# Kernel tuning notes

Hardware: AMD Instinct MI355X
Metric: run time of the kernel (lower is better)

The kernel has to match this reference:

```python
import jax, jax.numpy as jnp
import numpy as np

B, L, F, H, N_HASHES = 2, 2048, 1024, 16, 4
HD = F // H  # head_dim = 64


def setup_inputs() -> dict:
    key = jax.random.key(0)
    ks = jax.random.split(key, 8)
    s = 0.02
    return {
        "x": jax.random.normal(ks[0], (B, L, F), jnp.float32),
        "Wqk": jax.random.normal(ks[1], (F, 2 * F), jnp.float32) * s,
        "bqk": jnp.zeros((2 * F,), jnp.float32),
        "Wv": jax.random.normal(ks[2], (F, F), jnp.float32) * s,
        "bv": jnp.zeros((F,), jnp.float32),
        "Wo": jax.random.normal(ks[3], (F, F), jnp.float32) * s,
        "bo": jnp.zeros((F,), jnp.float32),
        "R": jax.random.normal(ks[4], (H, N_HASHES, HD), jnp.float32) * s,
    }


def reference(x, Wqk, bqk, Wv, bv, Wo, bo, R):
    b, l, f = x.shape
    h, _, hd = R.shape

    qk = x @ Wqk + bqk                      # [B,L,2F]
    q, k = jnp.split(qk, 2, axis=-1)
    v = x @ Wv + bv                         # [B,L,F]

    def to_heads(t):
        return t.reshape(b, l, h, hd).transpose(0, 2, 1, 3)  # [B,H,L,D]

    q, k, v = to_heads(q), to_heads(k), to_heads(v)

    # LSH hashing of queries: argmax over [rotated, -rotated]
    rotated = jnp.einsum('bhld,hrd->bhlr', q, R)             # [B,H,L,n_hashes]
    buckets = jnp.argmax(jnp.concatenate([rotated, -rotated], axis=-1), axis=-1)  # [B,H,L]

    # Sort sequence positions by bucket id (per batch/head)
    idx = jnp.argsort(buckets, axis=-1)                      # [B,H,L]

    def gather_l(t):
        return jnp.take_along_axis(t, idx[..., None], axis=2)

    sq, sk, sv = gather_l(q), gather_l(k), gather_l(v)

    # Full dense attention over the sorted sequence
    scale = 1.0 / np.sqrt(hd).astype(np.float32)
    dots = jnp.einsum('bhqd,bhkd->bhqk', sq, sk) * scale     # [B,H,L,L]
    attn = jax.nn.softmax(dots, axis=-1)
    out = jnp.einsum('bhqk,bhkd->bhqd', attn, sv)            # [B,H,L,D]

    # Scatter back to original order
    restore = jnp.argsort(idx, axis=-1)
    out = jnp.take_along_axis(out, restore[..., None], axis=2)
    out = out.transpose(0, 2, 1, 3).reshape(b, l, f)
    return out @ Wo + bo
```

## Files before the change

kernel.cpp:

```cpp
#include <hip/hip_runtime.h>


#define B_ 2
#define L_ 2048
#define F_ 1024
#define H_ 16
#define D_ 64
#define M_ 4096

typedef unsigned short u16;
typedef unsigned int   u32;
typedef __bf16 bf16x8 __attribute__((ext_vector_type(8)));
typedef float  f32x4  __attribute__((ext_vector_type(4)));

__device__ __forceinline__ u16 f2bf(float f) {
    __bf16 h = (__bf16)f;
    return __builtin_bit_cast(u16, h);
}

__device__ __forceinline__ void glds16(const void* g, void* l) {
    __builtin_amdgcn_global_load_lds(
        (const __attribute__((address_space(1))) u32*)g,
        (__attribute__((address_space(3))) u32*)l, 16, 0, 0);
}

#define MFMA16(a, b, c) __builtin_amdgcn_mfma_f32_16x16x32_bf16(a, b, c, 0, 0, 0)

__global__ __launch_bounds__(256) void cast_x(const float* __restrict__ x, u16* __restrict__ xb) {
    int i0 = blockIdx.x * 256 + threadIdx.x;
    #pragma unroll
    for (int r = 0; r < 4; ++r) {
        int i = i0 + r * 262144;
        float4 v = ((const float4*)x)[i];
        ushort4 o; o.x = f2bf(v.x); o.y = f2bf(v.y); o.z = f2bf(v.z); o.w = f2bf(v.w);
        ((ushort4*)xb)[i] = o;
    }
}

__global__ __launch_bounds__(256) void tr_all(
    const float* __restrict__ Wqk, const float* __restrict__ Wv,
    const float* __restrict__ Wo, u16* __restrict__ Wt, u16* __restrict__ Wot)
{
    __shared__ float tile[32][33];
    const int z = blockIdx.z;
    const float* src; u16* dst; int N;
    if (z == 0)      { src = Wqk; dst = Wt;                       N = 2048; }
    else if (z == 1) { src = Wv;  dst = Wt + (size_t)2048 * 1024; N = 1024; }
    else             { src = Wo;  dst = Wot;                      N = 1024; }
    int n0 = blockIdx.x * 32, k0 = blockIdx.y * 32;
    if (n0 >= N) return;
    int tx = threadIdx.x & 31, ty = threadIdx.x >> 5;
    #pragma unroll
    for (int i = 0; i < 4; ++i) {
        int k = ty + i * 8;
        tile[k][tx] = src[(size_t)(k0 + k) * N + n0 + tx];
    }
    __syncthreads();
    #pragma unroll
    for (int i = 0; i < 4; ++i) {
        int n = ty + i * 8;
        dst[(size_t)(n0 + n) * 1024 + k0 + tx] = f2bf(tile[tx][n]);
    }
}

__device__ __forceinline__ void gemm_loop(
    const u16* __restrict__ A, const u16* __restrict__ Bt,
    size_t m0, size_t n0, u16* As, u16* Bs, int t, f32x4 acc[4][4])
{
    const int w = t >> 6, lane = t & 63, ml = lane & 15, quad = lane >> 4;
    const int mw = (w >> 1) * 64, nw = (w & 1) * 64;
    const int srow = (lane >> 2), schunk = (lane & 3) * 8;

    for (int k0 = 0; k0 < 1024; k0 += 32) {
        __syncthreads();
        #pragma unroll
        for (int i = 0; i < 2; ++i) {
            int row = w * 32 + i * 16 + srow;
            glds16(A  + (m0 + row) * 1024 + k0 + schunk, As + (w * 32 + i * 16) * 32);
            glds16(Bt + (n0 + row) * 1024 + k0 + schunk, Bs + (w * 32 + i * 16) * 32);
        }
        __syncthreads();
        bf16x8 af[4], bf_[4];
        #pragma unroll
        for (int mt = 0; mt < 4; ++mt)
            af[mt] = *(const bf16x8*)(As + (mw + mt * 16 + ml) * 32 + quad * 8);
        #pragma unroll
        for (int nt = 0; nt < 4; ++nt)
            bf_[nt] = *(const bf16x8*)(Bs + (nw + nt * 16 + ml) * 32 + quad * 8);
        #pragma unroll
        for (int mt = 0; mt < 4; ++mt)
            #pragma unroll
            for (int nt = 0; nt < 4; ++nt)
                acc[mt][nt] = MFMA16(af[mt], bf_[nt], acc[mt][nt]);
    }
}

__global__ __launch_bounds__(256) void qkv_gemm(
    const u16* __restrict__ xb, const u16* __restrict__ Wt,
    const float* __restrict__ bqk, const float* __restrict__ bv,
    u16* __restrict__ Qb, u16* __restrict__ Kb, u16* __restrict__ Vt)
{
    __shared__ __align__(16) u16 As[128 * 32];
    __shared__ __align__(16) u16 Bs[128 * 32];
    const int t = threadIdx.x;
    const size_t m0 = blockIdx.y * 128, n0 = blockIdx.x * 128;
    f32x4 acc[4][4] = {};
    gemm_loop(xb, Wt, m0, n0, As, Bs, t, acc);

    const int w = t >> 6, lane = t & 63, ml = lane & 15, quad = lane >> 4;
    const int mw = (w >> 1) * 64, nw = (w & 1) * 64;
    const int seg = (int)(n0 >> 10);

    #pragma unroll
    for (int mt = 0; mt < 4; ++mt) {
        #pragma unroll
        for (int nt = 0; nt < 4; ++nt) {
            f32x4 a = acc[mt][nt];
            int c = (int)n0 + nw + nt * 16 + ml;
            int mbase = (int)m0 + mw + mt * 16 + quad * 4;
            if (seg == 2) {
                int cv = c - 2048, h = cv >> 6, d = cv & 63;
                float bias = bv[cv];
                int bb = mbase >> 11, l0 = mbase & (L_ - 1);
                int g = (l0 >> 2) & 15;
                int col = (l0 & ~63) + ((g & 8) << 2) + ((g & 3) << 3) + (g & 4);
                ushort4 pk;
                pk.x = f2bf(a[0] + bias); pk.y = f2bf(a[1] + bias);
                pk.z = f2bf(a[2] + bias); pk.w = f2bf(a[3] + bias);
                *(ushort4*)&Vt[(((size_t)(bb * H_ + h)) * D_ + d) * L_ + col] = pk;
            } else {
                float bias = bqk[c];
                float sc = (seg == 0) ? 0.1803368801111244f : 1.0f;
                u16* dst = (seg == 0) ? Qb : Kb;
                int cc = c & 1023, h = cc >> 6, d = cc & 63;
                #pragma unroll
                for (int reg = 0; reg < 4; ++reg) {
                    int m = mbase + reg, bb = m >> 11, l = m & (L_ - 1);
                    dst[(((size_t)(bb * H_ + h)) * L_ + l) * D_ + d] = f2bf((a[reg] + bias) * sc);
                }
            }
        }
    }
}

__global__ __launch_bounds__(256) void out_gemm(
    const u16* __restrict__ Ob, const u16* __restrict__ Wot,
    const float* __restrict__ bo, float* __restrict__ out)
{
    __shared__ __align__(16) u16 As[64 * 32];
    __shared__ __align__(16) u16 Bs[128 * 32];
    const int t = threadIdx.x, w = t >> 6, lane = t & 63;
    const int ml = lane & 15, quad = lane >> 4;
    const int mw = (w >> 1) * 32, nw = (w & 1) * 64;
    const size_t m0 = blockIdx.y * 64, n0 = blockIdx.x * 128;
    const int srow = lane >> 2, schunk = (lane & 3) * 8;

    f32x4 acc[2][4] = {};
    for (int k0 = 0; k0 < 1024; k0 += 32) {
        __syncthreads();
        {
            int row = w * 16 + srow;
            glds16(Ob + (m0 + row) * 1024 + k0 + schunk, As + (w * 16) * 32);
        }
        #pragma unroll
        for (int i = 0; i < 2; ++i) {
            int row = w * 32 + i * 16 + srow;
            glds16(Wot + (n0 + row) * 1024 + k0 + schunk, Bs + (w * 32 + i * 16) * 32);
        }
        __syncthreads();
        bf16x8 af[2], bf_[4];
        #pragma unroll
        for (int mt = 0; mt < 2; ++mt)
            af[mt] = *(const bf16x8*)(As + (mw + mt * 16 + ml) * 32 + quad * 8);
        #pragma unroll
        for (int nt = 0; nt < 4; ++nt)
            bf_[nt] = *(const bf16x8*)(Bs + (nw + nt * 16 + ml) * 32 + quad * 8);
        #pragma unroll
        for (int mt = 0; mt < 2; ++mt)
            #pragma unroll
            for (int nt = 0; nt < 4; ++nt)
                acc[mt][nt] = MFMA16(af[mt], bf_[nt], acc[mt][nt]);
    }

    #pragma unroll
    for (int mt = 0; mt < 2; ++mt)
        #pragma unroll
        for (int nt = 0; nt < 4; ++nt) {
            int c = (int)n0 + nw + nt * 16 + ml;
            int mbase = (int)m0 + mw + mt * 16 + quad * 4;
            float bias = bo[c];
            #pragma unroll
            for (int reg = 0; reg < 4; ++reg)
                out[(size_t)(mbase + reg) * F_ + c] = acc[mt][nt][reg] + bias;
        }
}

__global__ __launch_bounds__(256, 2) void attn_mfma(
    const u16* __restrict__ Qb, const u16* __restrict__ Kb,
    const u16* __restrict__ Vt, u16* __restrict__ Ob)
{
    __shared__ __align__(16) u16 smem[32768];

    const int t = threadIdx.x, w = t >> 6, lane = t & 63;
    const int ml = lane & 15, quad = lane >> 4;
    const int half = w >> 1, qsel = w & 1;
    const int qt = blockIdx.x, h = blockIdx.y, b = blockIdx.z;
    const int qbase = qt * 128 + qsel * 64;
    const size_t hoff = ((size_t)(b * H_ + h)) * L_ * D_;
    const u16* Qg = Qb + hoff;
    const u16* Kg = Kb + hoff;
    const u16* Vg = Vt + hoff;

    u16* Kbuf = smem + half * 8192;
    u16* Vbuf = smem + 16384 + half * 8192;

    bf16x8 qf[4][2];
    #pragma unroll
    for (int m2 = 0; m2 < 4; ++m2)
        #pragma unroll
        for (int k2 = 0; k2 < 2; ++k2)
            qf[m2][k2] = *(const bf16x8*)(Qg + (size_t)(qbase + m2 * 16 + ml) * 64 + k2 * 32 + quad * 8);

    const int srow = lane >> 3, sch = lane & 7;
    auto stage = [&](int i, int d) {
        int kt = half * 16 + i;
        #pragma unroll
        for (int ii = 0; ii < 4; ++ii) {
            int row = qsel * 32 + ii * 8 + srow;
            int ch = sch ^ (row & 7);
            glds16(Kg + (size_t)(kt * 64 + row) * 64 + ch * 8, Kbuf + d * 4096 + (qsel * 32 + ii * 8) * 64);
            glds16(Vg + (size_t)row * L_ + kt * 64 + ch * 8,   Vbuf + d * 4096 + (qsel * 32 + ii * 8) * 64);
        }
    };

    bf16x8 vone;
    #pragma unroll
    for (int j = 0; j < 8; ++j) vone[j] = (__bf16)1.0f;

    f32x4 oacc[4][5] = {};

    stage(0, 0);
    for (int i = 0; i < 16; ++i) {
        __syncthreads();
        if (i < 15) stage(i + 1, (i + 1) & 1);

        const u16* Kl = Kbuf + (i & 1) * 4096;
        const u16* Vl = Vbuf + (i & 1) * 4096;
        bf16x8 kf[4][2], vf[4][2];
        #pragma unroll
        for (int t4 = 0; t4 < 4; ++t4) {
            int row = t4 * 16 + ml;
            #pragma unroll
            for (int k2 = 0; k2 < 2; ++k2)
                kf[t4][k2] = *(const bf16x8*)(Kl + row * 64 + (((k2 * 4 + quad) ^ (row & 7)) << 3));
        }
        #pragma unroll
        for (int dt = 0; dt < 4; ++dt) {
            int row = dt * 16 + ml;
            #pragma unroll
            for (int tp = 0; tp < 2; ++tp)
                vf[dt][tp] = *(const bf16x8*)(Vl + row * 64 + (((tp * 4 + quad) ^ (row & 7)) << 3));
        }

        #pragma unroll
        for (int m2 = 0; m2 < 4; ++m2) {
            f32x4 sacc[4] = {};
            #pragma unroll
            for (int k2 = 0; k2 < 2; ++k2)
                #pragma unroll
                for (int t4 = 0; t4 < 4; ++t4)
                    sacc[t4] = MFMA16(kf[t4][k2], qf[m2][k2], sacc[t4]);

            bf16x8 ap[2];
            #pragma unroll
            for (int t4 = 0; t4 < 4; ++t4)
                #pragma unroll
                for (int r = 0; r < 4; ++r)
                    ap[t4 >> 1][(t4 & 1) * 4 + r] = (__bf16)exp2f(sacc[t4][r]);

            #pragma unroll
            for (int tp = 0; tp < 2; ++tp) {
                #pragma unroll
                for (int dt = 0; dt < 4; ++dt)
                    oacc[m2][dt] = MFMA16(ap[tp], vf[dt][tp], oacc[m2][dt]);
                oacc[m2][4] = MFMA16(ap[tp], vone, oacc[m2][4]);
            }
        }
    }

    __syncthreads();
    float* Fb = (float*)smem;
    if (half == 1) {
        #pragma unroll
        for (int m2 = 0; m2 < 4; ++m2)
            #pragma unroll
            for (int f = 0; f < 5; ++f)
                *(f32x4*)&Fb[(((qsel * 4 + m2) * 5 + f) * 64 + lane) * 4] = oacc[m2][f];
    }
    __syncthreads();
    if (half == 0) {
        #pragma unroll
        for (int m2 = 0; m2 < 4; ++m2)
            #pragma unroll
            for (int f = 0; f < 5; ++f)
                oacc[m2][f] += *(const f32x4*)&Fb[(((qsel * 4 + m2) * 5 + f) * 64 + lane) * 4];

        #pragma unroll
        for (int m2 = 0; m2 < 4; ++m2)
            #pragma unroll
            for (int r = 0; r < 4; ++r) {
                float il = 1.0f / oacc[m2][4][r];
                int row = b * L_ + qbase + m2 * 16 + quad * 4 + r;
                #pragma unroll
                for (int dt = 0; dt < 4; ++dt) {
                    int c = h * 64 + dt * 16 + ml;
                    Ob[(size_t)row * F_ + c] = f2bf(oacc[m2][dt][r] * il);
                }
            }
    }
}

extern "C" void kernel_launch(void* const* d_in, const int* in_sizes, int n_in,
                              void* d_out, int out_size, void* d_ws, size_t ws_size,
                              hipStream_t stream)
{
    const float* x   = (const float*)d_in[0];
    const float* Wqk = (const float*)d_in[1];
    const float* bqk = (const float*)d_in[2];
    const float* Wv  = (const float*)d_in[3];
    const float* bv  = (const float*)d_in[4];
    const float* Wo  = (const float*)d_in[5];
    const float* bo  = (const float*)d_in[6];
    (void)in_sizes; (void)n_in; (void)out_size; (void)ws_size;
    float* out = (float*)d_out;

    u16* w16 = (u16*)d_ws;
    u16* xb  = w16;
    u16* Wt  = xb  + 4194304;
    u16* Wot = Wt  + 3145728;
    u16* Qb  = Wot + 1048576;
    u16* Kb  = Qb  + 4194304;
    u16* Vtw = Kb  + 4194304;
    u16* Ob  = Vtw + 4194304;

    cast_x<<<1024, 256, 0, stream>>>(x, xb);
    tr_all<<<dim3(64, 32, 3), 256, 0, stream>>>(Wqk, Wv, Wo, Wt, Wot);
    qkv_gemm<<<dim3(24, 32), 256, 0, stream>>>(xb, Wt, bqk, bv, Qb, Kb, Vtw);
    attn_mfma<<<dim3(16, 16, 2), 256, 0, stream>>>(Qb, Kb, Vtw, Ob);
    out_gemm<<<dim3(8, 64), 256, 0, stream>>>(Ob, Wot, bo, out);
}
```

Measured before the change: 195.5 us.

## Shrink attention tiles, load V directly from global, raise occupancy

```diff
diff --git a/kernel.cpp b/kernel.cpp
--- a/kernel.cpp
+++ b/kernel.cpp
@@ -122,8 +122,7 @@
                 int cv = c - 2048, h = cv >> 6, d = cv & 63;
                 float bias = bv[cv];
                 int bb = mbase >> 11, l0 = mbase & (L_ - 1);
-                int g = (l0 >> 2) & 15;
-                int col = (l0 & ~63) + ((g & 8) << 2) + ((g & 3) << 3) + (g & 4);
+                int col = (l0 & ~31) + (((l0 >> 2) & 3) << 3) + (((l0 >> 4) & 1) << 2) + (l0 & 3);
                 ushort4 pk;
                 pk.x = f2bf(a[0] + bias); pk.y = f2bf(a[1] + bias);
                 pk.z = f2bf(a[2] + bias); pk.w = f2bf(a[3] + bias);
@@ -195,41 +194,38 @@
         }
 }
 
-__global__ __launch_bounds__(256, 2) void attn_mfma(
+__global__ __launch_bounds__(256, 4) void attn_mfma(
     const u16* __restrict__ Qb, const u16* __restrict__ Kb,
     const u16* __restrict__ Vt, u16* __restrict__ Ob)
 {
-    __shared__ __align__(16) u16 smem[32768];
+    __shared__ __align__(16) u16 smem[10240];
 
     const int t = threadIdx.x, w = t >> 6, lane = t & 63;
     const int ml = lane & 15, quad = lane >> 4;
     const int half = w >> 1, qsel = w & 1;
     const int qt = blockIdx.x, h = blockIdx.y, b = blockIdx.z;
-    const int qbase = qt * 128 + qsel * 64;
-    const size_t hoff = ((size_t)(b * H_ + h)) * L_ * D_;
+    const int qbase = qt * 64 + qsel * 32;
+    const size_t hoff = ((size_t)(b * H_ + h)) * (size_t)L_ * D_;
     const u16* Qg = Qb + hoff;
-    const u16* Kg = Kb + hoff;
+    const u16* Kg = Kb + hoff + (size_t)half * 1024 * 64;
     const u16* Vg = Vt + hoff;
-
-    u16* Kbuf = smem + half * 8192;
-    u16* Vbuf = smem + 16384 + half * 8192;
-
-    bf16x8 qf[4][2];
-    #pragma unroll
-    for (int m2 = 0; m2 < 4; ++m2)
+    u16* Kst = smem + half * 4096;
+
+    bf16x8 qf[2][2];
+    #pragma unroll
+    for (int m2 = 0; m2 < 2; ++m2)
         #pragma unroll
         for (int k2 = 0; k2 < 2; ++k2)
             qf[m2][k2] = *(const bf16x8*)(Qg + (size_t)(qbase + m2 * 16 + ml) * 64 + k2 * 32 + quad * 8);
 
     const int srow = lane >> 3, sch = lane & 7;
-    auto stage = [&](int i, int d) {
-        int kt = half * 16 + i;
-        #pragma unroll
-        for (int ii = 0; ii < 4; ++ii) {
-            int row = qsel * 32 + ii * 8 + srow;
+    auto stageK = [&](int i, int d) {
+        #pragma unroll
+        for (int ii = 0; ii < 2; ++ii) {
+            int row = qsel * 16 + ii * 8 + srow;
             int ch = sch ^ (row & 7);
-            glds16(Kg + (size_t)(kt * 64 + row) * 64 + ch * 8, Kbuf + d * 4096 + (qsel * 32 + ii * 8) * 64);
-            glds16(Vg + (size_t)row * L_ + kt * 64 + ch * 8,   Vbuf + d * 4096 + (qsel * 32 + ii * 8) * 64);
+            glds16(Kg + (size_t)(i * 32 + row) * 64 + ch * 8,
+                   Kst + d * 2048 + (qsel * 16 + ii * 8) * 64);
         }
     };
 
@@ -237,54 +233,50 @@
     #pragma unroll
     for (int j = 0; j < 8; ++j) vone[j] = (__bf16)1.0f;
 
-    f32x4 oacc[4][5] = {};
-
-    stage(0, 0);
-    for (int i = 0; i < 16; ++i) {
-        __syncthreads();
-        if (i < 15) stage(i + 1, (i + 1) & 1);
-
-        const u16* Kl = Kbuf + (i & 1) * 4096;
-        const u16* Vl = Vbuf + (i & 1) * 4096;
-        bf16x8 kf[4][2], vf[4][2];
-        #pragma unroll
-        for (int t4 = 0; t4 < 4; ++t4) {
+    f32x4 oacc[2][5] = {};
+    const u16* vbase = Vg + (size_t)ml * L_ + half * 1024 + quad * 8;
+
+    stageK(0, 0);
+    for (int i = 0; i < 32; ++i) {
+        __syncthreads();
+
+        bf16x8 vf[4];
+        #pragma unroll
+        for (int dt = 0; dt < 4; ++dt)
+            vf[dt] = *(const bf16x8*)(vbase + (size_t)dt * 16 * L_ + i * 32);
+
+        if (i < 31) stageK(i + 1, (i + 1) & 1);
+
+        const u16* Kl = Kst + (i & 1) * 2048;
+        bf16x8 kf[2][2];
+        #pragma unroll
+        for (int t4 = 0; t4 < 2; ++t4) {
             int row = t4 * 16 + ml;
             #pragma unroll
             for (int k2 = 0; k2 < 2; ++k2)
                 kf[t4][k2] = *(const bf16x8*)(Kl + row * 64 + (((k2 * 4 + quad) ^ (row & 7)) << 3));
         }
-        #pragma unroll
-        for (int dt = 0; dt < 4; ++dt) {
-            int row = dt * 16 + ml;
-            #pragma unroll
-            for (int tp = 0; tp < 2; ++tp)
-                vf[dt][tp] = *(const bf16x8*)(Vl + row * 64 + (((tp * 4 + quad) ^ (row & 7)) << 3));
-        }
-
-        #pragma unroll
-        for (int m2 = 0; m2 < 4; ++m2) {
-            f32x4 sacc[4] = {};
+
+        #pragma unroll
+        for (int m2 = 0; m2 < 2; ++m2) {
+            f32x4 sacc[2] = {};
             #pragma unroll
             for (int k2 = 0; k2 < 2; ++k2)
                 #pragma unroll
-                for (int t4 = 0; t4 < 4; ++t4)
+                for (int t4 = 0; t4 < 2; ++t4)
                     sacc[t4] = MFMA16(kf[t4][k2], qf[m2][k2], sacc[t4]);
 
-            bf16x8 ap[2];
-            #pragma unroll
-            for (int t4 = 0; t4 < 4; ++t4)
+            bf16x8 ap;
+            #pragma unroll
+            for (int t4 = 0; t4 < 2; ++t4)
                 #pragma unroll
                 for (int r = 0; r < 4; ++r)
-                    ap[t4 >> 1][(t4 & 1) * 4 + r] = (__bf16)exp2f(sacc[t4][r]);
-
-            #pragma unroll
-            for (int tp = 0; tp < 2; ++tp) {
-                #pragma unroll
-                for (int dt = 0; dt < 4; ++dt)
-                    oacc[m2][dt] = MFMA16(ap[tp], vf[dt][tp], oacc[m2][dt]);
-                oacc[m2][4] = MFMA16(ap[tp], vone, oacc[m2][4]);
-            }
+                    ap[t4 * 4 + r] = (__bf16)exp2f(sacc[t4][r]);
+
+            #pragma unroll
+            for (int dt = 0; dt < 4; ++dt)
+                oacc[m2][dt] = MFMA16(ap, vf[dt], oacc[m2][dt]);
+            oacc[m2][4] = MFMA16(ap, vone, oacc[m2][4]);
         }
     }
 
@@ -292,21 +284,21 @@
     float* Fb = (float*)smem;
     if (half == 1) {
         #pragma unroll
-        for (int m2 = 0; m2 < 4; ++m2)
+        for (int m2 = 0; m2 < 2; ++m2)
             #pragma unroll
             for (int f = 0; f < 5; ++f)
-                *(f32x4*)&Fb[(((qsel * 4 + m2) * 5 + f) * 64 + lane) * 4] = oacc[m2][f];
+                *(f32x4*)&Fb[(((qsel * 2 + m2) * 5 + f) * 64 + lane) * 4] = oacc[m2][f];
     }
     __syncthreads();
     if (half == 0) {
         #pragma unroll
-        for (int m2 = 0; m2 < 4; ++m2)
+        for (int m2 = 0; m2 < 2; ++m2)
             #pragma unroll
             for (int f = 0; f < 5; ++f)
-                oacc[m2][f] += *(const f32x4*)&Fb[(((qsel * 4 + m2) * 5 + f) * 64 + lane) * 4];
-
-        #pragma unroll
-        for (int m2 = 0; m2 < 4; ++m2)
+                oacc[m2][f] += *(const f32x4*)&Fb[(((qsel * 2 + m2) * 5 + f) * 64 + lane) * 4];
+
+        #pragma unroll
+        for (int m2 = 0; m2 < 2; ++m2)
             #pragma unroll
             for (int r = 0; r < 4; ++r) {
                 float il = 1.0f / oacc[m2][4][r];
@@ -346,6 +338,6 @@
     cast_x<<<1024, 256, 0, stream>>>(x, xb);
     tr_all<<<dim3(64, 32, 3), 256, 0, stream>>>(Wqk, Wv, Wo, Wt, Wot);
     qkv_gemm<<<dim3(24, 32), 256, 0, stream>>>(xb, Wt, bqk, bv, Qb, Kb, Vtw);
-    attn_mfma<<<dim3(16, 16, 2), 256, 0, stream>>>(Qb, Kb, Vtw, Ob);
+    attn_mfma<<<dim3(32, 16, 2), 256, 0, stream>>>(Qb, Kb, Vtw, Ob);
     out_gemm<<<dim3(8, 64), 256, 0, stream>>>(Ob, Wot, bo, out);
 }
```

Measured after the change: 217.2 us. 1.11x slower.
